# Optimization experiments

Measured on AMD Instinct MI355X. Metric: run time of the kernel, lower is better.

Reference implementation:

```python
import jax, jax.numpy as jnp
import numpy as np

N, E = 50000, 1600000
IN_CH, HEADS, OUT_PER_HEAD = 128, 4, 32  # out_channels=128 // 4 heads
NEG_SLOPE = 0.2


def setup_inputs() -> dict:
    key = jax.random.key(0)
    ks = jax.random.split(key, 10)
    HC = HEADS * OUT_PER_HEAD
    glorot = lambda k, shape: jax.random.uniform(k, shape, jnp.float32, -1.0, 1.0) * jnp.sqrt(6.0 / (shape[0] + shape[-1]))
    return {
        "x": jax.random.normal(ks[0], (N, IN_CH), jnp.float32),
        "edge_index": jax.random.randint(ks[1], (2, E), 0, N),
        "edge_weight": jax.random.uniform(ks[2], (E,), jnp.float32),
        "Wl": glorot(ks[3], (IN_CH, HC)),
        "bl": jnp.zeros((HC,), jnp.float32),
        "Wr": glorot(ks[4], (IN_CH, HC)),
        "br": jnp.zeros((HC,), jnp.float32),
        "We": glorot(ks[5], (1, HC)),           # lin_edge, bias=False
        "att": glorot(ks[6], (HEADS, OUT_PER_HEAD)),
        "bias": jnp.zeros((HC,), jnp.float32),
    }


def reference(x, edge_index, edge_weight, Wl, bl, Wr, br, We, att, bias):
    n = x.shape[0]
    H, C = att.shape
    src, dst = edge_index[0], edge_index[1]
    # add_self_loops with fill_value='max': self-loop edge_attr = max incoming edge weight per node (0 if none)
    loop_attr = jax.ops.segment_max(edge_weight, dst, num_segments=n)
    loop_attr = jnp.where(jnp.isfinite(loop_attr), loop_attr, 0.0)
    loop = jnp.arange(n)
    src_f = jnp.concatenate([src, loop])
    dst_f = jnp.concatenate([dst, loop])
    ea_f = jnp.concatenate([edge_weight, loop_attr])[:, None]  # [E+N, 1]
    # GATv2: separate src/dst linear transforms
    x_l = (x @ Wl + bl).reshape(n, H, C)
    x_r = (x @ Wr + br).reshape(n, H, C)
    e = (ea_f @ We).reshape(-1, H, C)
    # per-edge message and attention score
    m = jax.nn.leaky_relu(x_l[src_f] + x_r[dst_f] + e, NEG_SLOPE)  # [E+N, H, C]
    alpha = jnp.einsum('ehc,hc->eh', m, att)
    # scatter-softmax over incoming edges per destination node
    amax = jax.ops.segment_max(alpha, dst_f, num_segments=n)
    amax = jnp.where(jnp.isfinite(amax), amax, 0.0)
    aexp = jnp.exp(alpha - amax[dst_f])
    asum = jax.ops.segment_sum(aexp, dst_f, num_segments=n)
    alpha = aexp / (asum[dst_f] + 1e-16)
    # weighted aggregate of source-transformed features
    out = jax.ops.segment_sum(x_l[src_f] * alpha[..., None], dst_f, num_segments=n)
    return out.reshape(n, H * C) + bias
```

## Files before the change

### kernel.cpp

```cpp
#include <hip/hip_runtime.h>
#include <cstdint>

#define NEG 0.2f
#define BSH 4
#define BNODES 16
#define CAP 768
#define EPT 3
#define SBSH 9
#define SBN 512
#define CCAP 18000
#define LOG2E 1.44269504088896f

typedef __attribute__((ext_vector_type(8))) short short8v;
typedef __attribute__((ext_vector_type(4))) float f32x4;

__device__ __forceinline__ unsigned short f2bf(float f) {
  unsigned u = __float_as_uint(f);
  return (unsigned short)((u + 0x7FFFu + ((u >> 16) & 1u)) >> 16);
}

__global__ __launch_bounds__(256) void k_prep(const float* __restrict__ Wl,
    const float* __restrict__ Wr, unsigned short* __restrict__ WtB) {
  int mat = blockIdx.x;
  const float* W = mat ? Wr : Wl;
  for (int i = threadIdx.x; i < 16384; i += 256) {
    int c = i >> 7, k = i & 127;
    WtB[mat * 16384 + c * 128 + k] = f2bf(W[k * 128 + c]);
  }
}

__global__ __launch_bounds__(256) void k_gemm(const float* __restrict__ x,
    const unsigned short* __restrict__ WtB,
    const float* __restrict__ bl, const float* __restrict__ br,
    unsigned short* __restrict__ xlb, unsigned short* __restrict__ xrb, int n) {
  __shared__ __align__(16) unsigned short xs[64][136];
  __shared__ __align__(16) unsigned short Wt[128][136];
  int tid = threadIdx.x;
  int B0 = blockIdx.x * 64;
  for (int i = tid; i < 64 * 32; i += 256) {
    int r = i >> 5, c4 = (i & 31) * 4;
    ushort4 o = {0, 0, 0, 0};
    if (B0 + r < n) {
      float4 v = *(const float4*)(x + (size_t)(B0 + r) * 128 + c4);
      o = make_ushort4(f2bf(v.x), f2bf(v.y), f2bf(v.z), f2bf(v.w));
    }
    *(ushort4*)&xs[r][c4] = o;
  }
  int wv = tid >> 6, lane = tid & 63;
  int l15 = lane & 15, g = lane >> 4;
  int R0 = wv * 16;
  for (int mat = 0; mat < 2; ++mat) {
    __syncthreads();
    for (int i = tid; i < 128 * 32; i += 256) {
      int c = i >> 5, k4 = (i & 31) * 4;
      *(ushort4*)&Wt[c][k4] = *(const ushort4*)(WtB + (size_t)mat * 16384 + c * 128 + k4);
    }
    __syncthreads();
    f32x4 acc[8];
    #pragma unroll
    for (int t = 0; t < 8; ++t) acc[t] = {0.f, 0.f, 0.f, 0.f};
    #pragma unroll
    for (int kc = 0; kc < 4; ++kc) {
      int k0 = kc * 32 + g * 8;
      short8v a = *(const short8v*)&xs[R0 + l15][k0];
      #pragma unroll
      for (int t = 0; t < 8; ++t) {
        short8v b = *(const short8v*)&Wt[t * 16 + l15][k0];
        acc[t] = __builtin_amdgcn_mfma_f32_16x16x32_bf16(a, b, acc[t], 0, 0, 0);
      }
    }
    const float* bias = mat ? br : bl;
    unsigned short* yp = mat ? xrb : xlb;
    #pragma unroll
    for (int t = 0; t < 8; ++t) {
      int col = t * 16 + l15;
      float bv = bias[col];
      #pragma unroll
      for (int q = 0; q < 4; ++q) {
        int row = B0 + R0 + g * 4 + q;
        if (row < n) yp[(size_t)row * 128 + col] = f2bf(acc[t][q] + bv);
      }
    }
  }
}

__global__ __launch_bounds__(256) void k_coarse(const int* __restrict__ eidx,
    const float* __restrict__ ew, unsigned* __restrict__ gsb,
    int2* __restrict__ csb, int E, int NSB, int chunk) {
  __shared__ unsigned cnt[128];
  __shared__ unsigned base[128];
  int c0 = blockIdx.x * chunk;
  int c1 = min(E, c0 + chunk);
  if (c0 >= c1) return;
  for (int b = threadIdx.x; b < NSB; b += 256) cnt[b] = 0u;
  __syncthreads();
  for (int i = c0 + threadIdx.x; i < c1; i += 256)
    atomicAdd(&cnt[((unsigned)eidx[E + i]) >> SBSH], 1u);
  __syncthreads();
  for (int b = threadIdx.x; b < NSB; b += 256) {
    unsigned c = cnt[b];
    base[b] = c ? atomicAdd(&gsb[b], c) : 0u;
    cnt[b] = 0u;
  }
  __syncthreads();
  for (int i = c0 + threadIdx.x; i < c1; i += 256) {
    unsigned d = (unsigned)eidx[E + i];
    unsigned b = d >> SBSH;
    unsigned slot = base[b] + atomicAdd(&cnt[b], 1u);
    if (slot < CCAP)
      csb[(size_t)b * CCAP + slot] =
          make_int2((eidx[i] << SBSH) | (int)(d & (SBN - 1)), __float_as_int(ew[i]));
  }
}

__global__ __launch_bounds__(1024) void k_fine(const unsigned* __restrict__ gsb,
    const int2* __restrict__ csb, int2* __restrict__ ebkt,
    unsigned* __restrict__ fcnt, int NB) {
  __shared__ unsigned cnt[32];
  int sb = blockIdx.x;
  int ne = min((int)gsb[sb], CCAP);
  const int2* src = csb + (size_t)sb * CCAP;
  if (threadIdx.x < 32) cnt[threadIdx.x] = 0u;
  __syncthreads();
  for (int i = threadIdx.x; i < ne; i += 1024) {
    int2 e = src[i];
    int fb = (e.x >> 4) & 31;
    unsigned slot = atomicAdd(&cnt[fb], 1u);
    if (slot < CAP) {
      int packed = ((e.x >> SBSH) << 4) | (e.x & 15);
      ebkt[(size_t)(sb * 32 + fb) * CAP + slot] = make_int2(packed, e.y);
    }
  }
  __syncthreads();
  if (threadIdx.x < 32) {
    int fb = sb * 32 + (int)threadIdx.x;
    if (fb < NB) fcnt[fb] = min(cnt[threadIdx.x], (unsigned)CAP);
  }
}

__global__ __launch_bounds__(256) void k_agg(
    const unsigned* __restrict__ fcnt, const int2* __restrict__ ebkt,
    const unsigned short* __restrict__ xlb, const unsigned short* __restrict__ xrb,
    const float* __restrict__ We, const float* __restrict__ att,
    const float* __restrict__ bias, float* __restrict__ out, int n) {
  __shared__ int2 es[CAP];
  __shared__ unsigned rp[BNODES + 1];
  __shared__ unsigned cur[BNODES];
  __shared__ unsigned scnt[BNODES];
  int tid = threadIdx.x;
  int lane = tid & 63, wv = tid >> 6;
  int bkt = blockIdx.x;
  int ne = min((int)fcnt[bkt], CAP);
  const int2* srcp = ebkt + (size_t)bkt * CAP;
  if (tid < BNODES) scnt[tid] = 0u;
  __syncthreads();
  int2 er[EPT];
  #pragma unroll
  for (int k = 0; k < EPT; ++k) {
    int i = tid + k * 256;
    if (i < ne) {
      er[k] = srcp[i];
      atomicAdd(&scnt[er[k].x & (BNODES - 1)], 1u);
    }
  }
  __syncthreads();
  if (tid < 64) {
    unsigned s = (lane < BNODES) ? scnt[lane] : 0u;
    #pragma unroll
    for (int off = 1; off < BNODES; off <<= 1) {
      unsigned t = __shfl_up(s, off);
      if (lane >= off) s += t;
    }
    if (lane < BNODES) { rp[lane + 1] = s; cur[lane] = 0u; }
    if (lane == 0) rp[0] = 0u;
  }
  __syncthreads();
  #pragma unroll
  for (int k = 0; k < EPT; ++k) {
    int i = tid + k * 256;
    if (i < ne) {
      int dl = er[k].x & (BNODES - 1);
      unsigned slot = rp[dl] + atomicAdd(&cur[dl], 1u);
      es[slot] = make_int2(er[k].x >> BSH, er[k].y);
    }
  }
  __syncthreads();

  int g = lane >> 4;
  int l4 = lane & 15;
  int ch0 = l4 * 8;
  float4 weA = *(const float4*)(We + ch0);
  float4 weB = *(const float4*)(We + ch0 + 4);
  float4 atA = *(const float4*)(att + ch0);
  float4 atB = *(const float4*)(att + ch0 + 4);
  atA.x *= LOG2E; atA.y *= LOG2E; atA.z *= LOG2E; atA.w *= LOG2E;
  atB.x *= LOG2E; atB.y *= LOG2E; atB.z *= LOG2E; atB.w *= LOG2E;

  for (int dl = wv; dl < BNODES; dl += 4) {
    int d = (bkt << BSH) + dl;
    if (d >= n) break;
    int s0 = (int)rp[dl], s1 = (int)rp[dl + 1];
    uint4 xrq = *(const uint4*)(xrb + ((size_t)d << 7) + ch0);
    float4 xrA, xrB;
    xrA.x = __uint_as_float(xrq.x << 16);
    xrA.y = __uint_as_float(xrq.x & 0xFFFF0000u);
    xrA.z = __uint_as_float(xrq.y << 16);
    xrA.w = __uint_as_float(xrq.y & 0xFFFF0000u);
    xrB.x = __uint_as_float(xrq.z << 16);
    xrB.y = __uint_as_float(xrq.z & 0xFFFF0000u);
    xrB.z = __uint_as_float(xrq.w << 16);
    xrB.w = __uint_as_float(xrq.w & 0xFFFF0000u);
    float den = 0.f, wmax = -INFINITY;
    float4 aA = {0, 0, 0, 0}, aB = {0, 0, 0, 0};
    int idx = s0 + g;
    bool valid = idx < s1;
    int2 ev = make_int2(0, 0);
    uint4 xq = {0, 0, 0, 0};
    if (valid) {
      ev = es[idx];
      xq = *(const uint4*)(xlb + ((size_t)ev.x << 7) + ch0);
    }
    for (int j = s0; j < s1; j += 4) {
      int idxn = j + 4 + g;
      bool vn = idxn < s1;
      int2 evn = ev; uint4 xqn = xq;
      if (vn) {
        evn = es[idxn];
        xqn = *(const uint4*)(xlb + ((size_t)evn.x << 7) + ch0);
      }
      if (valid) {
        float w = __int_as_float(ev.y);
        wmax = fmaxf(wmax, w);
        float4 xA, xB;
        xA.x = __uint_as_float(xq.x << 16);
        xA.y = __uint_as_float(xq.x & 0xFFFF0000u);
        xA.z = __uint_as_float(xq.y << 16);
        xA.w = __uint_as_float(xq.y & 0xFFFF0000u);
        xB.x = __uint_as_float(xq.z << 16);
        xB.y = __uint_as_float(xq.z & 0xFFFF0000u);
        xB.z = __uint_as_float(xq.w << 16);
        xB.w = __uint_as_float(xq.w & 0xFFFF0000u);
        float4 tA, tB;
        tA.x = xA.x + xrA.x + w * weA.x;
        tA.y = xA.y + xrA.y + w * weA.y;
        tA.z = xA.z + xrA.z + w * weA.z;
        tA.w = xA.w + xrA.w + w * weA.w;
        tB.x = xB.x + xrB.x + w * weB.x;
        tB.y = xB.y + xrB.y + w * weB.y;
        tB.z = xB.z + xrB.z + w * weB.z;
        tB.w = xB.w + xrB.w + w * weB.w;
        tA.x = fmaxf(tA.x, NEG * tA.x);
        tA.y = fmaxf(tA.y, NEG * tA.y);
        tA.z = fmaxf(tA.z, NEG * tA.z);
        tA.w = fmaxf(tA.w, NEG * tA.w);
        tB.x = fmaxf(tB.x, NEG * tB.x);
        tB.y = fmaxf(tB.y, NEG * tB.y);
        tB.z = fmaxf(tB.z, NEG * tB.z);
        tB.w = fmaxf(tB.w, NEG * tB.w);
        float p = tA.x * atA.x + tA.y * atA.y + tA.z * atA.z + tA.w * atA.w
                + tB.x * atB.x + tB.y * atB.y + tB.z * atB.z + tB.w * atB.w;
        p += __shfl_xor(p, 1);
        p += __shfl_xor(p, 2);
        float pe = exp2f(p);
        den += pe;
        aA.x += pe * xA.x; aA.y += pe * xA.y; aA.z += pe * xA.z; aA.w += pe * xA.w;
        aB.x += pe * xB.x; aB.y += pe * xB.y; aB.z += pe * xB.z; aB.w += pe * xB.w;
      }
      ev = evn; xq = xqn; valid = vn;
    }
    #pragma unroll
    for (int mask = 16; mask <= 32; mask <<= 1) {
      den += __shfl_xor(den, mask);
      aA.x += __shfl_xor(aA.x, mask); aA.y += __shfl_xor(aA.y, mask);
      aA.z += __shfl_xor(aA.z, mask); aA.w += __shfl_xor(aA.w, mask);
      aB.x += __shfl_xor(aB.x, mask); aB.y += __shfl_xor(aB.y, mask);
      aB.z += __shfl_xor(aB.z, mask); aB.w += __shfl_xor(aB.w, mask);
      wmax = fmaxf(wmax, __shfl_xor(wmax, mask));
    }
    {
      float wl = (wmax > -INFINITY) ? wmax : 0.f;
      uint4 xq2 = *(const uint4*)(xlb + ((size_t)d << 7) + ch0);
      float4 xA, xB;
      xA.x = __uint_as_float(xq2.x << 16);
      xA.y = __uint_as_float(xq2.x & 0xFFFF0000u);
      xA.z = __uint_as_float(xq2.y << 16);
      xA.w = __uint_as_float(xq2.y & 0xFFFF0000u);
      xB.x = __uint_as_float(xq2.z << 16);
      xB.y = __uint_as_float(xq2.z & 0xFFFF0000u);
      xB.z = __uint_as_float(xq2.w << 16);
      xB.w = __uint_as_float(xq2.w & 0xFFFF0000u);
      float4 tA, tB;
      tA.x = xA.x + xrA.x + wl * weA.x;
      tA.y = xA.y + xrA.y + wl * weA.y;
      tA.z = xA.z + xrA.z + wl * weA.z;
      tA.w = xA.w + xrA.w + wl * weA.w;
      tB.x = xB.x + xrB.x + wl * weB.x;
      tB.y = xB.y + xrB.y + wl * weB.y;
      tB.z = xB.z + xrB.z + wl * weB.z;
      tB.w = xB.w + xrB.w + wl * weB.w;
      tA.x = fmaxf(tA.x, NEG * tA.x);
      tA.y = fmaxf(tA.y, NEG * tA.y);
      tA.z = fmaxf(tA.z, NEG * tA.z);
      tA.w = fmaxf(tA.w, NEG * tA.w);
      tB.x = fmaxf(tB.x, NEG * tB.x);
      tB.y = fmaxf(tB.y, NEG * tB.y);
      tB.z = fmaxf(tB.z, NEG * tB.z);
      tB.w = fmaxf(tB.w, NEG * tB.w);
      float p = tA.x * atA.x + tA.y * atA.y + tA.z * atA.z + tA.w * atA.w
              + tB.x * atB.x + tB.y * atB.y + tB.z * atB.z + tB.w * atB.w;
      p += __shfl_xor(p, 1);
      p += __shfl_xor(p, 2);
      float pe = exp2f(p);
      den += pe;
      aA.x += pe * xA.x; aA.y += pe * xA.y; aA.z += pe * xA.z; aA.w += pe * xA.w;
      aB.x += pe * xB.x; aB.y += pe * xB.y; aB.z += pe * xB.z; aB.w += pe * xB.w;
    }
    if (g == 0) {
      float r = 1.0f / den;
      float4 bvA = *(const float4*)(bias + ch0);
      float4 bvB = *(const float4*)(bias + ch0 + 4);
      float* op = out + (size_t)d * 128 + ch0;
      float4 oA = {aA.x * r + bvA.x, aA.y * r + bvA.y, aA.z * r + bvA.z, aA.w * r + bvA.w};
      float4 oB = {aB.x * r + bvB.x, aB.y * r + bvB.y, aB.z * r + bvB.z, aB.w * r + bvB.w};
      *(float4*)op = oA;
      *(float4*)(op + 4) = oB;
    }
  }
}

extern "C" void kernel_launch(void* const* d_in, const int* in_sizes, int n_in,
                              void* d_out, int out_size, void* d_ws, size_t ws_size,
                              hipStream_t stream) {
  const float* x     = (const float*)d_in[0];
  const int*   eidx  = (const int*)d_in[1];
  const float* ew_in = (const float*)d_in[2];
  const float* Wl    = (const float*)d_in[3];
  const float* bl    = (const float*)d_in[4];
  const float* Wr    = (const float*)d_in[5];
  const float* br    = (const float*)d_in[6];
  const float* We    = (const float*)d_in[7];
  const float* att   = (const float*)d_in[8];
  const float* bias  = (const float*)d_in[9];
  float* out = (float*)d_out;

  const int N = in_sizes[0] / 128;
  const int E = in_sizes[2];
  const int NB = (N + BNODES - 1) >> BSH;
  const int NSB = (N + SBN - 1) >> SBSH;

  char* ws = (char*)d_ws;
  size_t off = 0;
  auto alloc = [&](size_t bytes) {
    void* p = ws + off;
    off = (off + bytes + 255) & ~(size_t)255;
    return p;
  };
  int2* ebkt = (int2*)alloc((size_t)NB * CAP * 8);
  size_t ov_start = off;
  unsigned short* xlb = (unsigned short*)alloc((size_t)N * 128 * 2);
  unsigned short* xrb = (unsigned short*)alloc((size_t)N * 128 * 2);
  int2* csb = (int2*)(ws + ov_start);
  unsigned short* WtB = (unsigned short*)alloc(2 * 16384 * 2);
  unsigned* fcnt = (unsigned*)alloc((size_t)NB * 4);
  unsigned* gsb  = (unsigned*)alloc((size_t)NSB * 4);

  hipMemsetAsync(gsb, 0, (size_t)NSB * 4, stream);

  k_prep<<<2, 256, 0, stream>>>(Wl, Wr, WtB);

  int nblk = 512;
  int chunk = (E + nblk - 1) / nblk;
  k_coarse<<<nblk, 256, 0, stream>>>(eidx, ew_in, gsb, csb, E, NSB, chunk);

  k_fine<<<NSB, 1024, 0, stream>>>(gsb, csb, ebkt, fcnt, NB);

  k_gemm<<<(N + 63) / 64, 256, 0, stream>>>(x, WtB, bl, br, xlb, xrb, N);

  k_agg<<<NB, 256, 0, stream>>>(fcnt, ebkt, xlb, xrb, We, att, bias, out, N);
}
```

Before: 175.8 us.

## Split leaky-ReLU into linear plus abs terms with precomputed per-node attention projections

Rewrites leaky_relu(t) as 0.6*t + 0.4*|t|. The linear part of the attention score is then precomputed per node (ql, qr) inside the GEMM epilogue and per head for the edge weight (qe), so the per-edge work only evaluates the abs term. The aggregation kernel now has each lane cover 16 channels and handles 8 edges per wave iteration, which shortens the per-edge shuffle reduction. k_coarse is changed to a fixed chunk size per block and keeps destination indices in registers instead of reading them twice. This adds GEMM epilogue reductions, extra small buffers and more register pressure in k_agg.

```diff
diff --git a/kernel.cpp b/kernel.cpp
--- a/kernel.cpp
+++ b/kernel.cpp
@@ -9,6 +9,8 @@
 #define SBSH 9
 #define SBN 512
 #define CCAP 18000
+#define CCHUNK 3328
+#define CEPT 13
 #define LOG2E 1.44269504088896f
 
 typedef __attribute__((ext_vector_type(8))) short short8v;
@@ -20,19 +22,32 @@
 }
 
 __global__ __launch_bounds__(256) void k_prep(const float* __restrict__ Wl,
-    const float* __restrict__ Wr, unsigned short* __restrict__ WtB) {
+    const float* __restrict__ Wr, const float* __restrict__ We,
+    const float* __restrict__ att, unsigned short* __restrict__ WtB,
+    float* __restrict__ qe) {
   int mat = blockIdx.x;
   const float* W = mat ? Wr : Wl;
   for (int i = threadIdx.x; i < 16384; i += 256) {
     int c = i >> 7, k = i & 127;
     WtB[mat * 16384 + c * 128 + k] = f2bf(W[k * 128 + c]);
   }
+  if (mat == 0) {
+    __shared__ float tmp[128];
+    if (threadIdx.x < 128) tmp[threadIdx.x] = att[threadIdx.x] * We[threadIdx.x];
+    __syncthreads();
+    if (threadIdx.x < 4) {
+      float s = 0.f;
+      for (int c = 0; c < 32; ++c) s += tmp[threadIdx.x * 32 + c];
+      qe[threadIdx.x] = 0.6f * LOG2E * s;
+    }
+  }
 }
 
 __global__ __launch_bounds__(256) void k_gemm(const float* __restrict__ x,
-    const unsigned short* __restrict__ WtB,
+    const unsigned short* __restrict__ WtB, const float* __restrict__ att,
     const float* __restrict__ bl, const float* __restrict__ br,
-    unsigned short* __restrict__ xlb, unsigned short* __restrict__ xrb, int n) {
+    unsigned short* __restrict__ xlb, unsigned short* __restrict__ xrb,
+    float* __restrict__ ql, float* __restrict__ qr, int n) {
   __shared__ __align__(16) unsigned short xs[64][136];
   __shared__ __align__(16) unsigned short Wt[128][136];
   int tid = threadIdx.x;
@@ -49,6 +64,9 @@
   int wv = tid >> 6, lane = tid & 63;
   int l15 = lane & 15, g = lane >> 4;
   int R0 = wv * 16;
+  float attv[8];
+  #pragma unroll
+  for (int t = 0; t < 8; ++t) attv[t] = 0.6f * LOG2E * att[t * 16 + l15];
   for (int mat = 0; mat < 2; ++mat) {
     __syncthreads();
     for (int i = tid; i < 128 * 32; i += 256) {
@@ -71,31 +89,72 @@
     }
     const float* bias = mat ? br : bl;
     unsigned short* yp = mat ? xrb : xlb;
+    float* qdst = mat ? qr : ql;
+    float qp0[4] = {0, 0, 0, 0}, qp1[4] = {0, 0, 0, 0};
+    float qp2[4] = {0, 0, 0, 0}, qp3[4] = {0, 0, 0, 0};
     #pragma unroll
     for (int t = 0; t < 8; ++t) {
       int col = t * 16 + l15;
       float bv = bias[col];
+      float av = attv[t];
       #pragma unroll
       for (int q = 0; q < 4; ++q) {
         int row = B0 + R0 + g * 4 + q;
-        if (row < n) yp[(size_t)row * 128 + col] = f2bf(acc[t][q] + bv);
-      }
+        unsigned short hb = f2bf(acc[t][q] + bv);
+        if (row < n) yp[(size_t)row * 128 + col] = hb;
+        float fr = __uint_as_float(((unsigned)hb) << 16);
+        float c = av * fr;
+        if (q == 0) qp0[t >> 1] += c;
+        else if (q == 1) qp1[t >> 1] += c;
+        else if (q == 2) qp2[t >> 1] += c;
+        else qp3[t >> 1] += c;
+      }
+    }
+    #pragma unroll
+    for (int m2 = 1; m2 < 16; m2 <<= 1) {
+      #pragma unroll
+      for (int h2 = 0; h2 < 4; ++h2) {
+        qp0[h2] += __shfl_xor(qp0[h2], m2);
+        qp1[h2] += __shfl_xor(qp1[h2], m2);
+        qp2[h2] += __shfl_xor(qp2[h2], m2);
+        qp3[h2] += __shfl_xor(qp3[h2], m2);
+      }
+    }
+    if (l15 < 4) {
+      float v0 = (l15 == 0) ? qp0[0] : (l15 == 1) ? qp0[1] : (l15 == 2) ? qp0[2] : qp0[3];
+      float v1 = (l15 == 0) ? qp1[0] : (l15 == 1) ? qp1[1] : (l15 == 2) ? qp1[2] : qp1[3];
+      float v2 = (l15 == 0) ? qp2[0] : (l15 == 1) ? qp2[1] : (l15 == 2) ? qp2[2] : qp2[3];
+      float v3 = (l15 == 0) ? qp3[0] : (l15 == 1) ? qp3[1] : (l15 == 2) ? qp3[2] : qp3[3];
+      int rb = B0 + R0 + g * 4;
+      if (rb + 0 < n) qdst[(rb + 0) * 4 + l15] = v0;
+      if (rb + 1 < n) qdst[(rb + 1) * 4 + l15] = v1;
+      if (rb + 2 < n) qdst[(rb + 2) * 4 + l15] = v2;
+      if (rb + 3 < n) qdst[(rb + 3) * 4 + l15] = v3;
     }
   }
 }
 
 __global__ __launch_bounds__(256) void k_coarse(const int* __restrict__ eidx,
     const float* __restrict__ ew, unsigned* __restrict__ gsb,
-    int2* __restrict__ csb, int E, int NSB, int chunk) {
+    int2* __restrict__ csb, int E, int NSB) {
   __shared__ unsigned cnt[128];
   __shared__ unsigned base[128];
-  int c0 = blockIdx.x * chunk;
-  int c1 = min(E, c0 + chunk);
+  int c0 = blockIdx.x * CCHUNK;
+  int c1 = min(E, c0 + CCHUNK);
   if (c0 >= c1) return;
   for (int b = threadIdx.x; b < NSB; b += 256) cnt[b] = 0u;
   __syncthreads();
-  for (int i = c0 + threadIdx.x; i < c1; i += 256)
-    atomicAdd(&cnt[((unsigned)eidx[E + i]) >> SBSH], 1u);
+  unsigned dreg[CEPT];
+  #pragma unroll
+  for (int k = 0; k < CEPT; ++k) {
+    int i = c0 + threadIdx.x + k * 256;
+    unsigned d = 0u;
+    if (i < c1) {
+      d = (unsigned)eidx[E + i];
+      atomicAdd(&cnt[d >> SBSH], 1u);
+    }
+    dreg[k] = d;
+  }
   __syncthreads();
   for (int b = threadIdx.x; b < NSB; b += 256) {
     unsigned c = cnt[b];
@@ -103,13 +162,17 @@
     cnt[b] = 0u;
   }
   __syncthreads();
-  for (int i = c0 + threadIdx.x; i < c1; i += 256) {
-    unsigned d = (unsigned)eidx[E + i];
-    unsigned b = d >> SBSH;
-    unsigned slot = base[b] + atomicAdd(&cnt[b], 1u);
-    if (slot < CCAP)
-      csb[(size_t)b * CCAP + slot] =
-          make_int2((eidx[i] << SBSH) | (int)(d & (SBN - 1)), __float_as_int(ew[i]));
+  #pragma unroll
+  for (int k = 0; k < CEPT; ++k) {
+    int i = c0 + threadIdx.x + k * 256;
+    if (i < c1) {
+      unsigned d = dreg[k];
+      unsigned b = d >> SBSH;
+      unsigned slot = base[b] + atomicAdd(&cnt[b], 1u);
+      if (slot < CCAP)
+        csb[(size_t)b * CCAP + slot] =
+            make_int2((eidx[i] << SBSH) | (int)(d & (SBN - 1)), __float_as_int(ew[i]));
+    }
   }
 }
 
@@ -141,8 +204,10 @@
 __global__ __launch_bounds__(256) void k_agg(
     const unsigned* __restrict__ fcnt, const int2* __restrict__ ebkt,
     const unsigned short* __restrict__ xlb, const unsigned short* __restrict__ xrb,
-    const float* __restrict__ We, const float* __restrict__ att,
-    const float* __restrict__ bias, float* __restrict__ out, int n) {
+    const float* __restrict__ ql, const float* __restrict__ qr,
+    const float* __restrict__ qe, const float* __restrict__ We,
+    const float* __restrict__ att, const float* __restrict__ bias,
+    float* __restrict__ out, int n) {
   __shared__ int2 es[CAP];
   __shared__ unsigned rp[BNODES + 1];
   __shared__ unsigned cur[BNODES];
@@ -186,144 +251,137 @@
   }
   __syncthreads();
 
-  int g = lane >> 4;
-  int l4 = lane & 15;
-  int ch0 = l4 * 8;
-  float4 weA = *(const float4*)(We + ch0);
-  float4 weB = *(const float4*)(We + ch0 + 4);
-  float4 atA = *(const float4*)(att + ch0);
-  float4 atB = *(const float4*)(att + ch0 + 4);
-  atA.x *= LOG2E; atA.y *= LOG2E; atA.z *= LOG2E; atA.w *= LOG2E;
-  atB.x *= LOG2E; atB.y *= LOG2E; atB.z *= LOG2E; atB.w *= LOG2E;
+  int l8 = lane & 7, g3 = lane >> 3;
+  int ch0 = l8 * 16;
+  int h = l8 >> 1;
+  float wec[16], atc[16];
+  #pragma unroll
+  for (int k = 0; k < 4; ++k) {
+    float4 w4 = *(const float4*)(We + ch0 + k * 4);
+    wec[k * 4 + 0] = w4.x; wec[k * 4 + 1] = w4.y;
+    wec[k * 4 + 2] = w4.z; wec[k * 4 + 3] = w4.w;
+    float4 a4 = *(const float4*)(att + ch0 + k * 4);
+    atc[k * 4 + 0] = 0.4f * LOG2E * a4.x; atc[k * 4 + 1] = 0.4f * LOG2E * a4.y;
+    atc[k * 4 + 2] = 0.4f * LOG2E * a4.z; atc[k * 4 + 3] = 0.4f * LOG2E * a4.w;
+  }
+  float qeh = qe[h];
 
   for (int dl = wv; dl < BNODES; dl += 4) {
     int d = (bkt << BSH) + dl;
     if (d >= n) break;
     int s0 = (int)rp[dl], s1 = (int)rp[dl + 1];
-    uint4 xrq = *(const uint4*)(xrb + ((size_t)d << 7) + ch0);
-    float4 xrA, xrB;
-    xrA.x = __uint_as_float(xrq.x << 16);
-    xrA.y = __uint_as_float(xrq.x & 0xFFFF0000u);
-    xrA.z = __uint_as_float(xrq.y << 16);
-    xrA.w = __uint_as_float(xrq.y & 0xFFFF0000u);
-    xrB.x = __uint_as_float(xrq.z << 16);
-    xrB.y = __uint_as_float(xrq.z & 0xFFFF0000u);
-    xrB.z = __uint_as_float(xrq.w << 16);
-    xrB.w = __uint_as_float(xrq.w & 0xFFFF0000u);
+    float xrv[16];
+    {
+      uint4 a = *(const uint4*)(xrb + ((size_t)d << 7) + ch0);
+      uint4 b = *(const uint4*)(xrb + ((size_t)d << 7) + ch0 + 8);
+      xrv[0] = __uint_as_float(a.x << 16);  xrv[1] = __uint_as_float(a.x & 0xFFFF0000u);
+      xrv[2] = __uint_as_float(a.y << 16);  xrv[3] = __uint_as_float(a.y & 0xFFFF0000u);
+      xrv[4] = __uint_as_float(a.z << 16);  xrv[5] = __uint_as_float(a.z & 0xFFFF0000u);
+      xrv[6] = __uint_as_float(a.w << 16);  xrv[7] = __uint_as_float(a.w & 0xFFFF0000u);
+      xrv[8] = __uint_as_float(b.x << 16);  xrv[9] = __uint_as_float(b.x & 0xFFFF0000u);
+      xrv[10] = __uint_as_float(b.y << 16); xrv[11] = __uint_as_float(b.y & 0xFFFF0000u);
+      xrv[12] = __uint_as_float(b.z << 16); xrv[13] = __uint_as_float(b.z & 0xFFFF0000u);
+      xrv[14] = __uint_as_float(b.w << 16); xrv[15] = __uint_as_float(b.w & 0xFFFF0000u);
+    }
+    float qrd = qr[d * 4 + h];
+    float acc[16];
+    #pragma unroll
+    for (int k = 0; k < 16; ++k) acc[k] = 0.f;
     float den = 0.f, wmax = -INFINITY;
-    float4 aA = {0, 0, 0, 0}, aB = {0, 0, 0, 0};
-    int idx = s0 + g;
+    int idx = s0 + g3;
     bool valid = idx < s1;
     int2 ev = make_int2(0, 0);
-    uint4 xq = {0, 0, 0, 0};
+    uint4 xqa = {0, 0, 0, 0}, xqb = {0, 0, 0, 0};
+    float qls = 0.f;
     if (valid) {
       ev = es[idx];
-      xq = *(const uint4*)(xlb + ((size_t)ev.x << 7) + ch0);
-    }
-    for (int j = s0; j < s1; j += 4) {
-      int idxn = j + 4 + g;
+      xqa = *(const uint4*)(xlb + ((size_t)ev.x << 7) + ch0);
+      xqb = *(const uint4*)(xlb + ((size_t)ev.x << 7) + ch0 + 8);
+      qls = ql[ev.x * 4 + h];
+    }
+    for (int j = s0; j < s1; j += 8) {
+      int idxn = j + 8 + g3;
       bool vn = idxn < s1;
-      int2 evn = ev; uint4 xqn = xq;
+      int2 evn = ev; uint4 xan = xqa, xbn = xqb; float qln = qls;
       if (vn) {
         evn = es[idxn];
-        xqn = *(const uint4*)(xlb + ((size_t)evn.x << 7) + ch0);
+        xan = *(const uint4*)(xlb + ((size_t)evn.x << 7) + ch0);
+        xbn = *(const uint4*)(xlb + ((size_t)evn.x << 7) + ch0 + 8);
+        qln = ql[evn.x * 4 + h];
       }
       if (valid) {
         float w = __int_as_float(ev.y);
         wmax = fmaxf(wmax, w);
-        float4 xA, xB;
-        xA.x = __uint_as_float(xq.x << 16);
-        xA.y = __uint_as_float(xq.x & 0xFFFF0000u);
-        xA.z = __uint_as_float(xq.y << 16);
-        xA.w = __uint_as_float(xq.y & 0xFFFF0000u);
-        xB.x = __uint_as_float(xq.z << 16);
-        xB.y = __uint_as_float(xq.z & 0xFFFF0000u);
-        xB.z = __uint_as_float(xq.w << 16);
-        xB.w = __uint_as_float(xq.w & 0xFFFF0000u);
-        float4 tA, tB;
-        tA.x = xA.x + xrA.x + w * weA.x;
-        tA.y = xA.y + xrA.y + w * weA.y;
-        tA.z = xA.z + xrA.z + w * weA.z;
-        tA.w = xA.w + xrA.w + w * weA.w;
-        tB.x = xB.x + xrB.x + w * weB.x;
-        tB.y = xB.y + xrB.y + w * weB.y;
-        tB.z = xB.z + xrB.z + w * weB.z;
-        tB.w = xB.w + xrB.w + w * weB.w;
-        tA.x = fmaxf(tA.x, NEG * tA.x);
-        tA.y = fmaxf(tA.y, NEG * tA.y);
-        tA.z = fmaxf(tA.z, NEG * tA.z);
-        tA.w = fmaxf(tA.w, NEG * tA.w);
-        tB.x = fmaxf(tB.x, NEG * tB.x);
-        tB.y = fmaxf(tB.y, NEG * tB.y);
-        tB.z = fmaxf(tB.z, NEG * tB.z);
-        tB.w = fmaxf(tB.w, NEG * tB.w);
-        float p = tA.x * atA.x + tA.y * atA.y + tA.z * atA.z + tA.w * atA.w
-                + tB.x * atB.x + tB.y * atB.y + tB.z * atB.z + tB.w * atB.w;
-        p += __shfl_xor(p, 1);
-        p += __shfl_xor(p, 2);
-        float pe = exp2f(p);
+        float lin = qls + fmaf(w, qeh, qrd);
+        float xv[16];
+        xv[0] = __uint_as_float(xqa.x << 16);  xv[1] = __uint_as_float(xqa.x & 0xFFFF0000u);
+        xv[2] = __uint_as_float(xqa.y << 16);  xv[3] = __uint_as_float(xqa.y & 0xFFFF0000u);
+        xv[4] = __uint_as_float(xqa.z << 16);  xv[5] = __uint_as_float(xqa.z & 0xFFFF0000u);
+        xv[6] = __uint_as_float(xqa.w << 16);  xv[7] = __uint_as_float(xqa.w & 0xFFFF0000u);
+        xv[8] = __uint_as_float(xqb.x << 16);  xv[9] = __uint_as_float(xqb.x & 0xFFFF0000u);
+        xv[10] = __uint_as_float(xqb.y << 16); xv[11] = __uint_as_float(xqb.y & 0xFFFF0000u);
+        xv[12] = __uint_as_float(xqb.z << 16); xv[13] = __uint_as_float(xqb.z & 0xFFFF0000u);
+        xv[14] = __uint_as_float(xqb.w << 16); xv[15] = __uint_as_float(xqb.w & 0xFFFF0000u);
+        float nl = 0.f;
+        #pragma unroll
+        for (int k = 0; k < 16; ++k) {
+          float t = xv[k] + fmaf(w, wec[k], xrv[k]);
+          nl = fmaf(atc[k], fabsf(t), nl);
+        }
+        nl += __shfl_xor(nl, 1);
+        float pe = exp2f(lin + nl);
         den += pe;
-        aA.x += pe * xA.x; aA.y += pe * xA.y; aA.z += pe * xA.z; aA.w += pe * xA.w;
-        aB.x += pe * xB.x; aB.y += pe * xB.y; aB.z += pe * xB.z; aB.w += pe * xB.w;
-      }
-      ev = evn; xq = xqn; valid = vn;
-    }
-    #pragma unroll
-    for (int mask = 16; mask <= 32; mask <<= 1) {
+        #pragma unroll
+        for (int k = 0; k < 16; ++k) acc[k] = fmaf(pe, xv[k], acc[k]);
+      }
+      ev = evn; xqa = xan; xqb = xbn; qls = qln; valid = vn;
+    }
+    #pragma unroll
+    for (int mask = 8; mask <= 32; mask <<= 1) {
       den += __shfl_xor(den, mask);
-      aA.x += __shfl_xor(aA.x, mask); aA.y += __shfl_xor(aA.y, mask);
-      aA.z += __shfl_xor(aA.z, mask); aA.w += __shfl_xor(aA.w, mask);
-      aB.x += __shfl_xor(aB.x, mask); aB.y += __shfl_xor(aB.y, mask);
-      aB.z += __shfl_xor(aB.z, mask); aB.w += __shfl_xor(aB.w, mask);
+      #pragma unroll
+      for (int k = 0; k < 16; ++k) acc[k] += __shfl_xor(acc[k], mask);
       wmax = fmaxf(wmax, __shfl_xor(wmax, mask));
     }
     {
       float wl = (wmax > -INFINITY) ? wmax : 0.f;
-      uint4 xq2 = *(const uint4*)(xlb + ((size_t)d << 7) + ch0);
-      float4 xA, xB;
-      xA.x = __uint_as_float(xq2.x << 16);
-      xA.y = __uint_as_float(xq2.x & 0xFFFF0000u);
-      xA.z = __uint_as_float(xq2.y << 16);
-      xA.w = __uint_as_float(xq2.y & 0xFFFF0000u);
-      xB.x = __uint_as_float(xq2.z << 16);
-      xB.y = __uint_as_float(xq2.z & 0xFFFF0000u);
-      xB.z = __uint_as_float(xq2.w << 16);
-      xB.w = __uint_as_float(xq2.w & 0xFFFF0000u);
-      float4 tA, tB;
-      tA.x = xA.x + xrA.x + wl * weA.x;
-      tA.y = xA.y + xrA.y + wl * weA.y;
-      tA.z = xA.z + xrA.z + wl * weA.z;
-      tA.w = xA.w + xrA.w + wl * weA.w;
-      tB.x = xB.x + xrB.x + wl * weB.x;
-      tB.y = xB.y + xrB.y + wl * weB.y;
-      tB.z = xB.z + xrB.z + wl * weB.z;
-      tB.w = xB.w + xrB.w + wl * weB.w;
-      tA.x = fmaxf(tA.x, NEG * tA.x);
-      tA.y = fmaxf(tA.y, NEG * tA.y);
-      tA.z = fmaxf(tA.z, NEG * tA.z);
-      tA.w = fmaxf(tA.w, NEG * tA.w);
-      tB.x = fmaxf(tB.x, NEG * tB.x);
-      tB.y = fmaxf(tB.y, NEG * tB.y);
-      tB.z = fmaxf(tB.z, NEG * tB.z);
-      tB.w = fmaxf(tB.w, NEG * tB.w);
-      float p = tA.x * atA.x + tA.y * atA.y + tA.z * atA.z + tA.w * atA.w
-              + tB.x * atB.x + tB.y * atB.y + tB.z * atB.z + tB.w * atB.w;
-      p += __shfl_xor(p, 1);
-      p += __shfl_xor(p, 2);
-      float pe = exp2f(p);
+      uint4 a = *(const uint4*)(xlb + ((size_t)d << 7) + ch0);
+      uint4 b = *(const uint4*)(xlb + ((size_t)d << 7) + ch0 + 8);
+      float xv[16];
+      xv[0] = __uint_as_float(a.x << 16);  xv[1] = __uint_as_float(a.x & 0xFFFF0000u);
+      xv[2] = __uint_as_float(a.y << 16);  xv[3] = __uint_as_float(a.y & 0xFFFF0000u);
+      xv[4] = __uint_as_float(a.z << 16);  xv[5] = __uint_as_float(a.z & 0xFFFF0000u);
+      xv[6] = __uint_as_float(a.w << 16);  xv[7] = __uint_as_float(a.w & 0xFFFF0000u);
+      xv[8] = __uint_as_float(b.x << 16);  xv[9] = __uint_as_float(b.x & 0xFFFF0000u);
+      xv[10] = __uint_as_float(b.y << 16); xv[11] = __uint_as_float(b.y & 0xFFFF0000u);
+      xv[12] = __uint_as_float(b.z << 16); xv[13] = __uint_as_float(b.z & 0xFFFF0000u);
+      xv[14] = __uint_as_float(b.w << 16); xv[15] = __uint_as_float(b.w & 0xFFFF0000u);
+      float lin = ql[d * 4 + h] + fmaf(wl, qeh, qrd);
+      float nl = 0.f;
+      #pragma unroll
+      for (int k = 0; k < 16; ++k) {
+        float t = xv[k] + fmaf(wl, wec[k], xrv[k]);
+        nl = fmaf(atc[k], fabsf(t), nl);
+      }
+      nl += __shfl_xor(nl, 1);
+      float pe = exp2f(lin + nl);
       den += pe;
-      aA.x += pe * xA.x; aA.y += pe * xA.y; aA.z += pe * xA.z; aA.w += pe * xA.w;
-      aB.x += pe * xB.x; aB.y += pe * xB.y; aB.z += pe * xB.z; aB.w += pe * xB.w;
-    }
-    if (g == 0) {
+      #pragma unroll
+      for (int k = 0; k < 16; ++k) acc[k] = fmaf(pe, xv[k], acc[k]);
+    }
+    if (g3 == 0) {
       float r = 1.0f / den;
-      float4 bvA = *(const float4*)(bias + ch0);
-      float4 bvB = *(const float4*)(bias + ch0 + 4);
       float* op = out + (size_t)d * 128 + ch0;
-      float4 oA = {aA.x * r + bvA.x, aA.y * r + bvA.y, aA.z * r + bvA.z, aA.w * r + bvA.w};
-      float4 oB = {aB.x * r + bvB.x, aB.y * r + bvB.y, aB.z * r + bvB.z, aB.w * r + bvB.w};
-      *(float4*)op = oA;
-      *(float4*)(op + 4) = oB;
+      #pragma unroll
+      for (int k4 = 0; k4 < 4; ++k4) {
+        float4 bv = *(const float4*)(bias + ch0 + k4 * 4);
+        float4 o;
+        o.x = acc[k4 * 4 + 0] * r + bv.x;
+        o.y = acc[k4 * 4 + 1] * r + bv.y;
+        o.z = acc[k4 * 4 + 2] * r + bv.z;
+        o.w = acc[k4 * 4 + 3] * r + bv.w;
+        *(float4*)(op + k4 * 4) = o;
+      }
     }
   }
 }
@@ -361,20 +419,22 @@
   unsigned short* xrb = (unsigned short*)alloc((size_t)N * 128 * 2);
   int2* csb = (int2*)(ws + ov_start);
   unsigned short* WtB = (unsigned short*)alloc(2 * 16384 * 2);
+  float* ql = (float*)alloc((size_t)N * 4 * 4);
+  float* qr = (float*)alloc((size_t)N * 4 * 4);
+  float* qe = (float*)alloc(4 * 4);
   unsigned* fcnt = (unsigned*)alloc((size_t)NB * 4);
   unsigned* gsb  = (unsigned*)alloc((size_t)NSB * 4);
 
   hipMemsetAsync(gsb, 0, (size_t)NSB * 4, stream);
 
-  k_prep<<<2, 256, 0, stream>>>(Wl, Wr, WtB);
-
-  int nblk = 512;
-  int chunk = (E + nblk - 1) / nblk;
-  k_coarse<<<nblk, 256, 0, stream>>>(eidx, ew_in, gsb, csb, E, NSB, chunk);
+  k_prep<<<2, 256, 0, stream>>>(Wl, Wr, We, att, WtB, qe);
+
+  int nblk = (E + CCHUNK - 1) / CCHUNK;
+  k_coarse<<<nblk, 256, 0, stream>>>(eidx, ew_in, gsb, csb, E, NSB);
 
   k_fine<<<NSB, 1024, 0, stream>>>(gsb, csb, ebkt, fcnt, NB);
 
-  k_gemm<<<(N + 63) / 64, 256, 0, stream>>>(x, WtB, bl, br, xlb, xrb, N);
-
-  k_agg<<<NB, 256, 0, stream>>>(fcnt, ebkt, xlb, xrb, We, att, bias, out, N);
-}
+  k_gemm<<<(N + 63) / 64, 256, 0, stream>>>(x, WtB, att, bl, br, xlb, xrb, ql, qr, N);
+
+  k_agg<<<NB, 256, 0, stream>>>(fcnt, ebkt, xlb, xrb, ql, qr, qe, We, att, bias, out, N);
+}
```

Measured after the change: 180.4 us. 1.03x slower.

## Split GEMM across matrices in grid, vectorize stores, register-cache coarse bucketing

Applied to the files above, without the earlier changes.

The GEMM kernel now handles each of the two weight matrices in its own grid slice (blockIdx.y) instead of looping over both in one block. This doubles parallelism and removes a mid-kernel reload and barrier, at the cost of converting the x tile twice. The MFMA operands are swapped so each lane holds four contiguous output columns, which lets the epilogue use vectorized bias loads and ushort4 stores. The coarse edge bucketing kernel uses a fixed per-block chunk and keeps destination indices in registers, so it no longer reloads them in its second pass.

```diff
diff --git a/kernel.cpp b/kernel.cpp
--- a/kernel.cpp
+++ b/kernel.cpp
@@ -9,6 +9,8 @@
 #define SBSH 9
 #define SBN 512
 #define CCAP 18000
+#define CCHUNK 3328
+#define CEPT 13
 #define LOG2E 1.44269504088896f
 
 typedef __attribute__((ext_vector_type(8))) short short8v;
@@ -37,6 +39,7 @@
   __shared__ __align__(16) unsigned short Wt[128][136];
   int tid = threadIdx.x;
   int B0 = blockIdx.x * 64;
+  int mat = blockIdx.y;
   for (int i = tid; i < 64 * 32; i += 256) {
     int r = i >> 5, c4 = (i & 31) * 4;
     ushort4 o = {0, 0, 0, 0};
@@ -46,56 +49,63 @@
     }
     *(ushort4*)&xs[r][c4] = o;
   }
+  for (int i = tid; i < 128 * 32; i += 256) {
+    int c = i >> 5, k4 = (i & 31) * 4;
+    *(ushort4*)&Wt[c][k4] = *(const ushort4*)(WtB + (size_t)mat * 16384 + c * 128 + k4);
+  }
+  __syncthreads();
   int wv = tid >> 6, lane = tid & 63;
   int l15 = lane & 15, g = lane >> 4;
   int R0 = wv * 16;
-  for (int mat = 0; mat < 2; ++mat) {
-    __syncthreads();
-    for (int i = tid; i < 128 * 32; i += 256) {
-      int c = i >> 5, k4 = (i & 31) * 4;
-      *(ushort4*)&Wt[c][k4] = *(const ushort4*)(WtB + (size_t)mat * 16384 + c * 128 + k4);
-    }
-    __syncthreads();
-    f32x4 acc[8];
-    #pragma unroll
-    for (int t = 0; t < 8; ++t) acc[t] = {0.f, 0.f, 0.f, 0.f};
-    #pragma unroll
-    for (int kc = 0; kc < 4; ++kc) {
-      int k0 = kc * 32 + g * 8;
-      short8v a = *(const short8v*)&xs[R0 + l15][k0];
-      #pragma unroll
-      for (int t = 0; t < 8; ++t) {
-        short8v b = *(const short8v*)&Wt[t * 16 + l15][k0];
-        acc[t] = __builtin_amdgcn_mfma_f32_16x16x32_bf16(a, b, acc[t], 0, 0, 0);
-      }
-    }
-    const float* bias = mat ? br : bl;
-    unsigned short* yp = mat ? xrb : xlb;
+  f32x4 acc[8];
+  #pragma unroll
+  for (int t = 0; t < 8; ++t) acc[t] = {0.f, 0.f, 0.f, 0.f};
+  #pragma unroll
+  for (int kc = 0; kc < 4; ++kc) {
+    int k0 = kc * 32 + g * 8;
+    short8v b = *(const short8v*)&xs[R0 + l15][k0];
     #pragma unroll
     for (int t = 0; t < 8; ++t) {
-      int col = t * 16 + l15;
-      float bv = bias[col];
-      #pragma unroll
-      for (int q = 0; q < 4; ++q) {
-        int row = B0 + R0 + g * 4 + q;
-        if (row < n) yp[(size_t)row * 128 + col] = f2bf(acc[t][q] + bv);
-      }
+      short8v a = *(const short8v*)&Wt[t * 16 + l15][k0];
+      acc[t] = __builtin_amdgcn_mfma_f32_16x16x32_bf16(a, b, acc[t], 0, 0, 0);
+    }
+  }
+  const float* bias = mat ? br : bl;
+  unsigned short* yp = mat ? xrb : xlb;
+  int row = B0 + R0 + l15;
+  if (row < n) {
+    #pragma unroll
+    for (int t = 0; t < 8; ++t) {
+      int c0 = t * 16 + g * 4;
+      float4 bv = *(const float4*)(bias + c0);
+      ushort4 o = {f2bf(acc[t][0] + bv.x), f2bf(acc[t][1] + bv.y),
+                   f2bf(acc[t][2] + bv.z), f2bf(acc[t][3] + bv.w)};
+      *(ushort4*)(yp + (size_t)row * 128 + c0) = o;
     }
   }
 }
 
 __global__ __launch_bounds__(256) void k_coarse(const int* __restrict__ eidx,
     const float* __restrict__ ew, unsigned* __restrict__ gsb,
-    int2* __restrict__ csb, int E, int NSB, int chunk) {
+    int2* __restrict__ csb, int E, int NSB) {
   __shared__ unsigned cnt[128];
   __shared__ unsigned base[128];
-  int c0 = blockIdx.x * chunk;
-  int c1 = min(E, c0 + chunk);
+  int c0 = blockIdx.x * CCHUNK;
+  int c1 = min(E, c0 + CCHUNK);
   if (c0 >= c1) return;
   for (int b = threadIdx.x; b < NSB; b += 256) cnt[b] = 0u;
   __syncthreads();
-  for (int i = c0 + threadIdx.x; i < c1; i += 256)
-    atomicAdd(&cnt[((unsigned)eidx[E + i]) >> SBSH], 1u);
+  unsigned dreg[CEPT];
+  #pragma unroll
+  for (int k = 0; k < CEPT; ++k) {
+    int i = c0 + threadIdx.x + k * 256;
+    unsigned d = 0u;
+    if (i < c1) {
+      d = (unsigned)eidx[E + i];
+      atomicAdd(&cnt[d >> SBSH], 1u);
+    }
+    dreg[k] = d;
+  }
   __syncthreads();
   for (int b = threadIdx.x; b < NSB; b += 256) {
     unsigned c = cnt[b];
@@ -103,13 +113,17 @@
     cnt[b] = 0u;
   }
   __syncthreads();
-  for (int i = c0 + threadIdx.x; i < c1; i += 256) {
-    unsigned d = (unsigned)eidx[E + i];
-    unsigned b = d >> SBSH;
-    unsigned slot = base[b] + atomicAdd(&cnt[b], 1u);
-    if (slot < CCAP)
-      csb[(size_t)b * CCAP + slot] =
-          make_int2((eidx[i] << SBSH) | (int)(d & (SBN - 1)), __float_as_int(ew[i]));
+  #pragma unroll
+  for (int k = 0; k < CEPT; ++k) {
+    int i = c0 + threadIdx.x + k * 256;
+    if (i < c1) {
+      unsigned d = dreg[k];
+      unsigned b = d >> SBSH;
+      unsigned slot = base[b] + atomicAdd(&cnt[b], 1u);
+      if (slot < CCAP)
+        csb[(size_t)b * CCAP + slot] =
+            make_int2((eidx[i] << SBSH) | (int)(d & (SBN - 1)), __float_as_int(ew[i]));
+    }
   }
 }
 
@@ -368,13 +382,12 @@
 
   k_prep<<<2, 256, 0, stream>>>(Wl, Wr, WtB);
 
-  int nblk = 512;
-  int chunk = (E + nblk - 1) / nblk;
-  k_coarse<<<nblk, 256, 0, stream>>>(eidx, ew_in, gsb, csb, E, NSB, chunk);
+  int nblk = (E + CCHUNK - 1) / CCHUNK;
+  k_coarse<<<nblk, 256, 0, stream>>>(eidx, ew_in, gsb, csb, E, NSB);
 
   k_fine<<<NSB, 1024, 0, stream>>>(gsb, csb, ebkt, fcnt, NB);
 
-  k_gemm<<<(N + 63) / 64, 256, 0, stream>>>(x, WtB, bl, br, xlb, xrb, N);
+  k_gemm<<<dim3((N + 63) / 64, 2), 256, 0, stream>>>(x, WtB, bl, br, xlb, xrb, N);
 
   k_agg<<<NB, 256, 0, stream>>>(fcnt, ebkt, xlb, xrb, We, att, bias, out, N);
 }
```

Measured after the change: 165.3 us. -5.9%, faster.
